# Performance work log

Hardware: AMD Instinct MI355X
Metric: run time of the kernel (lower is better)

The kernel has to match this reference:

```python
import jax, jax.numpy as jnp
import numpy as np
from jax import lax

SR = 44100  # sample_rate from __init__ default


def _log_scale(v, mn, mx):
    # Faithful to AudioParameter.validate_and_scale with scale='log':
    # clamp, map log(v) to [0,1] over [log(mn), log(mx)], then rescale LINEARLY to [mn, mx].
    v = float(np.clip(float(v), mn, mx))
    log_min = np.log(max(mn, 1e-6))
    log_max = np.log(mx)
    normalized = (np.log(max(v, 1e-6)) - log_min) / (log_max - log_min)
    return normalized * (mx - mn) + mn


def _eq_coeffs(frequency, gain, q, sr=SR):
    # Parameter validation/scaling (frequency, q are 'log' scale; gain is linear clamp)
    f = _log_scale(frequency, 20.0, 20000.0)
    g = float(np.clip(float(gain), -30.0, 30.0))
    Q = _log_scale(q, 0.1, 30.0)
    # torchaudio.functional.equalizer_biquad ('bell' peaking EQ) coefficients
    w0 = 2.0 * np.pi * f / sr
    A = 10.0 ** (g / 40.0)
    alpha = np.sin(w0) / (2.0 * Q)
    b0 = 1.0 + alpha * A
    b1 = -2.0 * np.cos(w0)
    b2 = 1.0 - alpha * A
    a0 = 1.0 + alpha / A
    a1 = b1
    a2 = 1.0 - alpha / A
    return (b0 / a0, b1 / a0, b2 / a0, a1 / a0, a2 / a0)


def _biquad(x, coefs):
    # Direct-form-I second-order IIR along last axis, vectorized over all leading dims.
    b0, b1, b2, a1, a2 = [jnp.asarray(c, x.dtype) for c in coefs]
    shp = x.shape
    xf = x.reshape(-1, shp[-1])  # (N, T)
    z = jnp.zeros((xf.shape[0],), x.dtype)

    def step(carry, xn):
        x1, x2, y1, y2 = carry
        yn = b0 * xn + b1 * x1 + b2 * x2 - a1 * y1 - a2 * y2
        return (xn, x1, yn, y1), yn

    _, ys = lax.scan(step, (z, z, z, z), xf.T)  # ys: (T, N)
    return ys.T.reshape(shp)


def setup_inputs() -> dict:
    key = jax.random.key(0)
    audio = jax.random.normal(key, (32, 2, 441000), dtype=jnp.float32)  # 10s stereo, batch 32
    return {"audio": audio, "frequency": 2000, "gain": 6, "q": 1}


def reference(audio, frequency, gain, q):
    # filter_type='bell' (default) -> torchaudio equalizer_biquad path
    coefs = _eq_coeffs(frequency, gain, q)
    return _biquad(audio, coefs)
```

## Files before the change

### kernel.cpp

```cpp
#include <hip/hip_runtime.h>
#include <math.h>

#ifndef M_PI
#define M_PI 3.14159265358979323846
#endif

#define T_LEN      441000
#define L          16
#define WARM_LANES 16
#define OUT_W      ((64 - WARM_LANES) * L)
#define WPC        ((T_LEN + OUT_W - 1) / OUT_W)
#define BLOCK      256
#define BLK_X      ((WPC + 3) / 4)


__device__ __forceinline__ double log_scale(double v, double mn, double mx) {
    v = fmin(fmax(v, mn), mx);
    double lmin = log(fmax(mn, 1e-6));
    double lmax = log(mx);
    double nrm = (log(fmax(v, 1e-6)) - lmin) / (lmax - lmin);
    return nrm * (mx - mn) + mn;
}

__global__ void eq_setup_kernel(const int* __restrict__ f_in,
                                const int* __restrict__ g_in,
                                const int* __restrict__ q_in,
                                float* __restrict__ ws) {
    double f = log_scale((double)f_in[0], 20.0, 20000.0);
    double g = fmin(fmax((double)g_in[0], -30.0), 30.0);
    double Q = log_scale((double)q_in[0], 0.1, 30.0);
    double w0 = 2.0 * M_PI * f / 44100.0;
    double A  = pow(10.0, g / 40.0);
    double al = sin(w0) / (2.0 * Q);
    double ca = cos(w0);
    double b0 = 1.0 + al * A;
    double b1 = -2.0 * ca;
    double b2 = 1.0 - al * A;
    double a0 = 1.0 + al / A;
    double B0 = b0 / a0, B1 = b1 / a0, B2 = b2 / a0;
    double A1 = b1 / a0, A2 = (1.0 - al / A) / a0;
    ws[0] = (float)B0; ws[1] = (float)B1; ws[2] = (float)B2;
    ws[3] = (float)A1; ws[4] = (float)A2;

    const double m11 = -A1, m12 = -A2, m21 = 1.0, m22 = 0.0;

    double p11 = m11, p12 = m12, p21 = m21, p22 = m22;
    for (int i = 0; i < 4; ++i) {
        double s11 = p11 * p11 + p12 * p21;
        double s12 = p11 * p12 + p12 * p22;
        double s21 = p21 * p11 + p22 * p21;
        double s22 = p21 * p12 + p22 * p22;
        p11 = s11; p12 = s12; p21 = s21; p22 = s22;
    }
    for (int j = 0; j < 6; ++j) {
        ws[5 + 4 * j + 0] = (float)p11;
        ws[5 + 4 * j + 1] = (float)p12;
        ws[5 + 4 * j + 2] = (float)p21;
        ws[5 + 4 * j + 3] = (float)p22;
        double s11 = p11 * p11 + p12 * p21;
        double s12 = p11 * p12 + p12 * p22;
        double s21 = p21 * p11 + p22 * p21;
        double s22 = p21 * p12 + p22 * p22;
        p11 = s11; p12 = s12; p21 = s21; p22 = s22;
    }

    double q11 = m11, q12 = m12, q21 = m21, q22 = m22;
    for (int k = 0; k < 16; ++k) {
        ws[29 + 2 * k] = (float)q11;
        ws[30 + 2 * k] = (float)q12;
        const double n11 = m11 * q11 + m12 * q21;
        const double n12 = m11 * q12 + m12 * q22;
        const double n21 = q11;
        const double n22 = q12;
        q11 = n11; q12 = n12; q21 = n21; q22 = n22;
    }
}

__global__ __launch_bounds__(BLOCK, 6) void eq_main_kernel(
        const float* __restrict__ x,
        const float* __restrict__ ws,
        float* __restrict__ y) {
    const int tid  = threadIdx.x;
    const int lane = tid & 63;
    const int wv   = tid >> 6;
    const int wave = blockIdx.x * (BLOCK / 64) + wv;
    if (wave >= WPC) return;
    const int ch = blockIdx.y;

    const float b0 = ws[0], b1 = ws[1], b2 = ws[2], a1 = ws[3], a2 = ws[4];

    const float* __restrict__ xc = x + (size_t)ch * T_LEN;
    float*       __restrict__ yc = y + (size_t)ch * T_LEN;

    const int base = wave * OUT_W - WARM_LANES * L + lane * L;

    float xv[L], xm1, xm2;
    if (base >= 4 && base + L <= T_LEN) {
        const float4 vm = *reinterpret_cast<const float4*>(xc + base - 4);
        xm2 = vm.z; xm1 = vm.w;
        const float4 v0 = *reinterpret_cast<const float4*>(xc + base + 0);
        const float4 v1 = *reinterpret_cast<const float4*>(xc + base + 4);
        const float4 v2 = *reinterpret_cast<const float4*>(xc + base + 8);
        const float4 v3 = *reinterpret_cast<const float4*>(xc + base + 12);
        xv[0]=v0.x;  xv[1]=v0.y;  xv[2]=v0.z;  xv[3]=v0.w;
        xv[4]=v1.x;  xv[5]=v1.y;  xv[6]=v1.z;  xv[7]=v1.w;
        xv[8]=v2.x;  xv[9]=v2.y;  xv[10]=v2.z; xv[11]=v2.w;
        xv[12]=v3.x; xv[13]=v3.y; xv[14]=v3.z; xv[15]=v3.w;
    } else {
#pragma unroll
        for (int k = 0; k < L; ++k) {
            const int idx = base + k;
            xv[k] = (idx >= 0 && idx < T_LEN) ? xc[idx] : 0.f;
        }
        xm1 = (base - 1 >= 0 && base - 1 < T_LEN) ? xc[base - 1] : 0.f;
        xm2 = (base - 2 >= 0 && base - 2 < T_LEN) ? xc[base - 2] : 0.f;
    }

    float yl[L];
    float c0 = 0.f, c1 = 0.f;
    {
        float xk1 = xm1, xk2 = xm2;
#pragma unroll
        for (int k = 0; k < L; ++k) {
            const float xk = xv[k];
            const float t  = fmaf(b0, xk, fmaf(b1, xk1, b2 * xk2));
            const float yn = fmaf(-a1, c0, fmaf(-a2, c1, t));
            c1 = c0; c0 = yn;
            xk2 = xk1; xk1 = xk;
            yl[k] = yn;
        }
    }

#pragma unroll
    for (int j = 0; j < 6; ++j) {
        const float m11 = ws[5 + 4 * j + 0], m12 = ws[5 + 4 * j + 1];
        const float m21 = ws[5 + 4 * j + 2], m22 = ws[5 + 4 * j + 3];
        const float d0 = __shfl_up(c0, 1u << j);
        const float d1 = __shfl_up(c1, 1u << j);
        if (lane >= (1 << j)) {
            c0 = fmaf(m11, d0, fmaf(m12, d1, c0));
            c1 = fmaf(m21, d0, fmaf(m22, d1, c1));
        }
    }

    float s0 = __shfl_up(c0, 1);
    float s1 = __shfl_up(c1, 1);
    if (lane == 0) { s0 = 0.f; s1 = 0.f; }

    if (lane >= WARM_LANES && base < T_LEN) {
        if (base + L <= T_LEN) {
#pragma unroll
            for (int q = 0; q < L / 4; ++q) {
                float o[4];
#pragma unroll
                for (int r = 0; r < 4; ++r) {
                    const int k = 4 * q + r;
                    o[r] = fmaf(ws[29 + 2 * k], s0, fmaf(ws[30 + 2 * k], s1, yl[k]));
                }
                *reinterpret_cast<float4*>(yc + base + 4 * q) =
                    make_float4(o[0], o[1], o[2], o[3]);
            }
        } else {
#pragma unroll
            for (int k = 0; k < L; ++k)
                if (base + k < T_LEN)
                    yc[base + k] = fmaf(ws[29 + 2 * k], s0, fmaf(ws[30 + 2 * k], s1, yl[k]));
        }
    }
}

extern "C" void kernel_launch(void* const* d_in, const int* in_sizes, int n_in,
                              void* d_out, int out_size, void* d_ws, size_t ws_size,
                              hipStream_t stream) {
    const float* x = (const float*)d_in[0];
    const int*   f = (const int*)d_in[1];
    const int*   g = (const int*)d_in[2];
    const int*   q = (const int*)d_in[3];
    float*       y  = (float*)d_out;
    float*       ws = (float*)d_ws;

    eq_setup_kernel<<<1, 1, 0, stream>>>(f, g, q, ws);

    const int nch = in_sizes[0] / T_LEN;
    dim3 grid(BLK_X, nch);
    eq_main_kernel<<<grid, dim3(BLOCK), 0, stream>>>(x, ws, y);
}
```

Measured before the change: 215.4 us.

## Stage chunks through swizzled LDS for coalesced loads/stores, double per-lane length

Each wave now loads its input span with fully coalesced float4 reads into XOR-swizzled shared memory, then transposes it so each lane holds 32 contiguous samples. Outputs go back through LDS the same way for coalesced stores. Per-lane chunk length doubles to 32 and the warm-up region shrinks to 8 rows, which cuts redundant warm-up reads and compute. The costs are higher register pressure (occupancy hint lowered to 4) and extra LDS traffic, and the shorter warm-up relies on the filter's impulse response decaying within 256 samples.

Measured after the change: 213.0 us. No clear change (-1.1%).

```diff
diff --git a/kernel.cpp b/kernel.cpp
--- a/kernel.cpp
+++ b/kernel.cpp
@@ -6,12 +6,14 @@
 #endif
 
 #define T_LEN      441000
-#define L          16
-#define WARM_LANES 16
-#define OUT_W      ((64 - WARM_LANES) * L)
+#define L          32
+#define WARM_ROWS  8
+#define ROWS       64
+#define OUT_W      ((ROWS - WARM_ROWS) * L)
 #define WPC        ((T_LEN + OUT_W - 1) / OUT_W)
 #define BLOCK      256
-#define BLK_X      ((WPC + 3) / 4)
+#define WAVES_PB   (BLOCK / 64)
+#define BLK_X      ((WPC + WAVES_PB - 1) / WAVES_PB)
 
 
 __device__ __forceinline__ double log_scale(double v, double mn, double mx) {
@@ -45,7 +47,7 @@
     const double m11 = -A1, m12 = -A2, m21 = 1.0, m22 = 0.0;
 
     double p11 = m11, p12 = m12, p21 = m21, p22 = m22;
-    for (int i = 0; i < 4; ++i) {
+    for (int i = 0; i < 5; ++i) {
         double s11 = p11 * p11 + p12 * p21;
         double s12 = p11 * p12 + p12 * p22;
         double s21 = p21 * p11 + p22 * p21;
@@ -65,61 +67,77 @@
     }
 
     double q11 = m11, q12 = m12, q21 = m21, q22 = m22;
-    for (int k = 0; k < 16; ++k) {
+    for (int k = 0; k < L; ++k) {
         ws[29 + 2 * k] = (float)q11;
         ws[30 + 2 * k] = (float)q12;
         const double n11 = m11 * q11 + m12 * q21;
         const double n12 = m11 * q12 + m12 * q22;
-        const double n21 = q11;
-        const double n22 = q12;
-        q11 = n11; q12 = n12; q21 = n21; q22 = n22;
-    }
-}
-
-__global__ __launch_bounds__(BLOCK, 6) void eq_main_kernel(
+        q21 = q11; q22 = q12;
+        q11 = n11; q12 = n12;
+    }
+}
+
+__global__ __launch_bounds__(BLOCK, 4) void eq_main_kernel(
         const float* __restrict__ x,
         const float* __restrict__ ws,
         float* __restrict__ y) {
+    __shared__ float4 smem[WAVES_PB][ROWS * 8];
+
     const int tid  = threadIdx.x;
     const int lane = tid & 63;
     const int wv   = tid >> 6;
-    const int wave = blockIdx.x * (BLOCK / 64) + wv;
+    const int wave = blockIdx.x * WAVES_PB + wv;
     if (wave >= WPC) return;
     const int ch = blockIdx.y;
 
-    const float b0 = ws[0], b1 = ws[1], b2 = ws[2], a1 = ws[3], a2 = ws[4];
-
     const float* __restrict__ xc = x + (size_t)ch * T_LEN;
     float*       __restrict__ yc = y + (size_t)ch * T_LEN;
 
-    const int base = wave * OUT_W - WARM_LANES * L + lane * L;
-
-    float xv[L], xm1, xm2;
-    if (base >= 4 && base + L <= T_LEN) {
-        const float4 vm = *reinterpret_cast<const float4*>(xc + base - 4);
-        xm2 = vm.z; xm1 = vm.w;
-        const float4 v0 = *reinterpret_cast<const float4*>(xc + base + 0);
-        const float4 v1 = *reinterpret_cast<const float4*>(xc + base + 4);
-        const float4 v2 = *reinterpret_cast<const float4*>(xc + base + 8);
-        const float4 v3 = *reinterpret_cast<const float4*>(xc + base + 12);
-        xv[0]=v0.x;  xv[1]=v0.y;  xv[2]=v0.z;  xv[3]=v0.w;
-        xv[4]=v1.x;  xv[5]=v1.y;  xv[6]=v1.z;  xv[7]=v1.w;
-        xv[8]=v2.x;  xv[9]=v2.y;  xv[10]=v2.z; xv[11]=v2.w;
-        xv[12]=v3.x; xv[13]=v3.y; xv[14]=v3.z; xv[15]=v3.w;
-    } else {
-#pragma unroll
-        for (int k = 0; k < L; ++k) {
-            const int idx = base + k;
-            xv[k] = (idx >= 0 && idx < T_LEN) ? xc[idx] : 0.f;
-        }
-        xm1 = (base - 1 >= 0 && base - 1 < T_LEN) ? xc[base - 1] : 0.f;
-        xm2 = (base - 2 >= 0 && base - 2 < T_LEN) ? xc[base - 2] : 0.f;
-    }
+    const int obase = wave * OUT_W;
+    const int wbase = obase - WARM_ROWS * L;
+    float4* S = smem[wv];
+
+#pragma unroll
+    for (int c = 0; c < 8; ++c) {
+        const int q  = (c << 6) + lane;
+        const int g0 = wbase + (q << 2);
+        float4 v;
+        if (g0 >= 0 && g0 + 4 <= T_LEN) {
+            v = *reinterpret_cast<const float4*>(xc + g0);
+        } else {
+            float e[4];
+#pragma unroll
+            for (int j = 0; j < 4; ++j) {
+                const int idx = g0 + j;
+                e[j] = (idx >= 0 && idx < T_LEN) ? xc[idx] : 0.f;
+            }
+            v = make_float4(e[0], e[1], e[2], e[3]);
+        }
+        const int rr = q >> 3;
+        const int ck = q & 7;
+        S[(rr << 3) + (ck ^ (rr & 7))] = v;
+    }
+
+    float xv[L];
+#pragma unroll
+    for (int c = 0; c < 8; ++c) {
+        const float4 v = S[(lane << 3) + (c ^ (lane & 7))];
+        xv[4 * c + 0] = v.x; xv[4 * c + 1] = v.y;
+        xv[4 * c + 2] = v.z; xv[4 * c + 3] = v.w;
+    }
+    float pm1 = __shfl_up(xv[31], 1);
+    float pm2 = __shfl_up(xv[30], 1);
+    if (lane == 0) {
+        pm1 = (wbase - 1 >= 0) ? xc[wbase - 1] : 0.f;
+        pm2 = (wbase - 2 >= 0) ? xc[wbase - 2] : 0.f;
+    }
+
+    const float b0 = ws[0], b1 = ws[1], b2 = ws[2], a1 = ws[3], a2 = ws[4];
 
     float yl[L];
     float c0 = 0.f, c1 = 0.f;
     {
-        float xk1 = xm1, xk2 = xm2;
+        float xk1 = pm1, xk2 = pm2;
 #pragma unroll
         for (int k = 0; k < L; ++k) {
             const float xk = xv[k];
@@ -147,24 +165,30 @@
     float s1 = __shfl_up(c1, 1);
     if (lane == 0) { s0 = 0.f; s1 = 0.f; }
 
-    if (lane >= WARM_LANES && base < T_LEN) {
-        if (base + L <= T_LEN) {
-#pragma unroll
-            for (int q = 0; q < L / 4; ++q) {
-                float o[4];
-#pragma unroll
-                for (int r = 0; r < 4; ++r) {
-                    const int k = 4 * q + r;
-                    o[r] = fmaf(ws[29 + 2 * k], s0, fmaf(ws[30 + 2 * k], s1, yl[k]));
-                }
-                *reinterpret_cast<float4*>(yc + base + 4 * q) =
-                    make_float4(o[0], o[1], o[2], o[3]);
-            }
-        } else {
-#pragma unroll
-            for (int k = 0; k < L; ++k)
-                if (base + k < T_LEN)
-                    yc[base + k] = fmaf(ws[29 + 2 * k], s0, fmaf(ws[30 + 2 * k], s1, yl[k]));
+#pragma unroll
+    for (int c = 0; c < 8; ++c) {
+        float o[4];
+#pragma unroll
+        for (int r = 0; r < 4; ++r) {
+            const int k = 4 * c + r;
+            o[r] = fmaf(ws[29 + 2 * k], s0, fmaf(ws[30 + 2 * k], s1, yl[k]));
+        }
+        S[(lane << 3) + (c ^ (lane & 7))] = make_float4(o[0], o[1], o[2], o[3]);
+    }
+
+#pragma unroll
+    for (int c = 0; c < 7; ++c) {
+        const int q  = (c << 6) + lane;
+        const int rr = WARM_ROWS + (q >> 3);
+        const float4 o = S[(rr << 3) + ((q & 7) ^ (rr & 7))];
+        const int g0 = obase + (q << 2);
+        if (g0 + 4 <= T_LEN) {
+            *reinterpret_cast<float4*>(yc + g0) = o;
+        } else if (g0 < T_LEN) {
+            const float e[4] = {o.x, o.y, o.z, o.w};
+#pragma unroll
+            for (int j = 0; j < 4; ++j)
+                if (g0 + j < T_LEN) yc[g0 + j] = e[j];
         }
     }
 }
```

## Process two chained tiles per wave to amortize warmup overlap

Applied to the files above, without the earlier changes.

Each wave now scans two consecutive 1024-sample tiles, passing the final biquad state from the first tile into the second through the M^16 transition matrix. Only the first tile needs warmup lanes, so redundant reads and recomputation fall from a quarter of the work to about an eighth. Both tiles are loaded up front, which raises register use; the occupancy hint is lowered from 6 to 4 blocks accordingly.

Result: no change. 217.0 us (+0.7%).

```diff
diff --git a/kernel.cpp b/kernel.cpp
--- a/kernel.cpp
+++ b/kernel.cpp
@@ -7,9 +7,11 @@
 
 #define T_LEN      441000
 #define L          16
-#define WARM_LANES 16
-#define OUT_W      ((64 - WARM_LANES) * L)
-#define WPC        ((T_LEN + OUT_W - 1) / OUT_W)
+#define TILE       (64 * L)
+#define WARM       256
+#define WARM_LN    (WARM / L)
+#define CHAIN_OUT  (2 * TILE - WARM)
+#define WPC        ((T_LEN + CHAIN_OUT - 1) / CHAIN_OUT)
 #define BLOCK      256
 #define BLK_X      ((WPC + 3) / 4)
 
@@ -42,9 +44,9 @@
     ws[0] = (float)B0; ws[1] = (float)B1; ws[2] = (float)B2;
     ws[3] = (float)A1; ws[4] = (float)A2;
 
-    const double m11 = -A1, m12 = -A2, m21 = 1.0, m22 = 0.0;
-
-    double p11 = m11, p12 = m12, p21 = m21, p22 = m22;
+    const double m11 = -A1, m12 = -A2;
+
+    double p11 = m11, p12 = m12, p21 = 1.0, p22 = 0.0;
     for (int i = 0; i < 4; ++i) {
         double s11 = p11 * p11 + p12 * p21;
         double s12 = p11 * p12 + p12 * p22;
@@ -64,57 +66,53 @@
         p11 = s11; p12 = s12; p21 = s21; p22 = s22;
     }
 
-    double q11 = m11, q12 = m12, q21 = m21, q22 = m22;
-    for (int k = 0; k < 16; ++k) {
+    double q11 = m11, q12 = m12, q21 = 1.0, q22 = 0.0;
+    for (int k = 0; k < L; ++k) {
         ws[29 + 2 * k] = (float)q11;
         ws[30 + 2 * k] = (float)q12;
         const double n11 = m11 * q11 + m12 * q21;
         const double n12 = m11 * q12 + m12 * q22;
-        const double n21 = q11;
-        const double n22 = q12;
-        q11 = n11; q12 = n12; q21 = n21; q22 = n22;
-    }
-}
-
-__global__ __launch_bounds__(BLOCK, 6) void eq_main_kernel(
-        const float* __restrict__ x,
-        const float* __restrict__ ws,
-        float* __restrict__ y) {
-    const int tid  = threadIdx.x;
-    const int lane = tid & 63;
-    const int wv   = tid >> 6;
-    const int wave = blockIdx.x * (BLOCK / 64) + wv;
-    if (wave >= WPC) return;
-    const int ch = blockIdx.y;
-
+        q21 = q11; q22 = q12;
+        q11 = n11; q12 = n12;
+    }
+}
+
+__device__ __forceinline__ void load_tile(const float* __restrict__ xc, int base,
+                                          float4& vm, float4& v0, float4& v1,
+                                          float4& v2, float4& v3) {
+    if (base >= 4 && base + L <= T_LEN) {
+        vm = *reinterpret_cast<const float4*>(xc + base - 4);
+        v0 = *reinterpret_cast<const float4*>(xc + base + 0);
+        v1 = *reinterpret_cast<const float4*>(xc + base + 4);
+        v2 = *reinterpret_cast<const float4*>(xc + base + 8);
+        v3 = *reinterpret_cast<const float4*>(xc + base + 12);
+    } else {
+        float e[20];
+#pragma unroll
+        for (int k = 0; k < 20; ++k) {
+            const int idx = base - 4 + k;
+            e[k] = (idx >= 0 && idx < T_LEN) ? xc[idx] : 0.f;
+        }
+        vm = make_float4(e[0],  e[1],  e[2],  e[3]);
+        v0 = make_float4(e[4],  e[5],  e[6],  e[7]);
+        v1 = make_float4(e[8],  e[9],  e[10], e[11]);
+        v2 = make_float4(e[12], e[13], e[14], e[15]);
+        v3 = make_float4(e[16], e[17], e[18], e[19]);
+    }
+}
+
+__device__ __forceinline__ void tile_pass(const float* __restrict__ ws, int lane,
+        float4 vm, float4 v0, float4 v1, float4 v2, float4 v3,
+        bool first, float& g0, float& g1,
+        float* __restrict__ yc, int base, bool gate) {
     const float b0 = ws[0], b1 = ws[1], b2 = ws[2], a1 = ws[3], a2 = ws[4];
 
-    const float* __restrict__ xc = x + (size_t)ch * T_LEN;
-    float*       __restrict__ yc = y + (size_t)ch * T_LEN;
-
-    const int base = wave * OUT_W - WARM_LANES * L + lane * L;
-
-    float xv[L], xm1, xm2;
-    if (base >= 4 && base + L <= T_LEN) {
-        const float4 vm = *reinterpret_cast<const float4*>(xc + base - 4);
-        xm2 = vm.z; xm1 = vm.w;
-        const float4 v0 = *reinterpret_cast<const float4*>(xc + base + 0);
-        const float4 v1 = *reinterpret_cast<const float4*>(xc + base + 4);
-        const float4 v2 = *reinterpret_cast<const float4*>(xc + base + 8);
-        const float4 v3 = *reinterpret_cast<const float4*>(xc + base + 12);
-        xv[0]=v0.x;  xv[1]=v0.y;  xv[2]=v0.z;  xv[3]=v0.w;
-        xv[4]=v1.x;  xv[5]=v1.y;  xv[6]=v1.z;  xv[7]=v1.w;
-        xv[8]=v2.x;  xv[9]=v2.y;  xv[10]=v2.z; xv[11]=v2.w;
-        xv[12]=v3.x; xv[13]=v3.y; xv[14]=v3.z; xv[15]=v3.w;
-    } else {
-#pragma unroll
-        for (int k = 0; k < L; ++k) {
-            const int idx = base + k;
-            xv[k] = (idx >= 0 && idx < T_LEN) ? xc[idx] : 0.f;
-        }
-        xm1 = (base - 1 >= 0 && base - 1 < T_LEN) ? xc[base - 1] : 0.f;
-        xm2 = (base - 2 >= 0 && base - 2 < T_LEN) ? xc[base - 2] : 0.f;
-    }
+    float xv[L];
+    xv[0]=v0.x;  xv[1]=v0.y;  xv[2]=v0.z;  xv[3]=v0.w;
+    xv[4]=v1.x;  xv[5]=v1.y;  xv[6]=v1.z;  xv[7]=v1.w;
+    xv[8]=v2.x;  xv[9]=v2.y;  xv[10]=v2.z; xv[11]=v2.w;
+    xv[12]=v3.x; xv[13]=v3.y; xv[14]=v3.z; xv[15]=v3.w;
+    const float xm2 = vm.z, xm1 = vm.w;
 
     float yl[L];
     float c0 = 0.f, c1 = 0.f;
@@ -129,6 +127,12 @@
             xk2 = xk1; xk1 = xk;
             yl[k] = yn;
         }
+    }
+
+    if (!first && lane == 0) {
+        const float n0 = fmaf(ws[5], g0, fmaf(ws[6], g1, c0));
+        const float n1 = fmaf(ws[7], g0, fmaf(ws[8], g1, c1));
+        c0 = n0; c1 = n1;
     }
 
 #pragma unroll
@@ -143,11 +147,13 @@
         }
     }
 
+    const float ng0 = __shfl(c0, 63), ng1 = __shfl(c1, 63);
     float s0 = __shfl_up(c0, 1);
     float s1 = __shfl_up(c1, 1);
-    if (lane == 0) { s0 = 0.f; s1 = 0.f; }
-
-    if (lane >= WARM_LANES && base < T_LEN) {
+    if (lane == 0) { s0 = first ? 0.f : g0; s1 = first ? 0.f : g1; }
+    g0 = ng0; g1 = ng1;
+
+    if (gate && base < T_LEN) {
         if (base + L <= T_LEN) {
 #pragma unroll
             for (int q = 0; q < L / 4; ++q) {
@@ -167,6 +173,32 @@
                     yc[base + k] = fmaf(ws[29 + 2 * k], s0, fmaf(ws[30 + 2 * k], s1, yl[k]));
         }
     }
+}
+
+__global__ __launch_bounds__(BLOCK, 4) void eq_main_kernel(
+        const float* __restrict__ x,
+        const float* __restrict__ ws,
+        float* __restrict__ y) {
+    const int tid   = threadIdx.x;
+    const int lane  = tid & 63;
+    const int wv    = tid >> 6;
+    const int chain = blockIdx.x * (BLOCK / 64) + wv;
+    if (chain >= WPC) return;
+    const int ch = blockIdx.y;
+
+    const float* __restrict__ xc = x + (size_t)ch * T_LEN;
+    float*       __restrict__ yc = y + (size_t)ch * T_LEN;
+
+    const int base0 = chain * CHAIN_OUT - WARM + lane * L;
+    const int base1 = base0 + TILE;
+
+    float4 Am, A0, A1, A2, A3, Bm, B0, B1, B2, B3;
+    load_tile(xc, base0, Am, A0, A1, A2, A3);
+    load_tile(xc, base1, Bm, B0, B1, B2, B3);
+
+    float g0 = 0.f, g1 = 0.f;
+    tile_pass(ws, lane, Am, A0, A1, A2, A3, true,  g0, g1, yc, base0, lane >= WARM_LN);
+    tile_pass(ws, lane, Bm, B0, B1, B2, B3, false, g0, g1, yc, base1, true);
 }
 
 extern "C" void kernel_launch(void* const* d_in, const int* in_sizes, int n_in,
```
